# Performance work log

Hardware: AMD Instinct MI355X
Metric: run time of the kernel (lower is better)

Reference implementation:

```python
import jax, jax.numpy as jnp
import numpy as np

B = 256
D = 2048          # in_channels (shared latent dim)
S = 8             # n_subjects
OUT = 1000        # sum of 7 Schaefer network head widths [150,148,132,136,76,122,236]


def setup_inputs() -> dict:
    key = jax.random.key(0)
    k1, k2, k3, k4 = jax.random.split(key, 4)
    x = jax.random.normal(k1, (B, D), dtype=jnp.float32)
    subject_ids = jax.random.randint(k2, (B,), 0, S, dtype=jnp.int64)
    scale = 1.0 / np.sqrt(D)  # matches normal_(0, 1/in_channels**0.5)
    # Concatenated per-head weights: equivalent to 7 heads of shapes
    # (S, D, n_k) concatenated along the output axis (n_k sums to OUT).
    W = jax.random.normal(k3, (S, D, OUT), dtype=jnp.float32) * scale
    b = jax.random.normal(k4, (S, OUT), dtype=jnp.float32) * scale
    return {"x": x, "subject_ids": subject_ids, "W": W, "b": b}


def reference(x, subject_ids, W, b):
    # Per-sample weight gather (B, D, OUT) followed by batched matmul,
    # exactly mirroring torch: w = weights[subject_ids]; einsum('bd,bdo->bo').
    w = W[subject_ids]                      # (B, D, OUT) gathered copy
    out = jnp.einsum('bd,bdo->bo', x, w)    # (B, OUT)
    out = out + b[subject_ids]              # per-subject bias
    return out
```

## Files before the change

### kernel.cpp

```cpp
#include <hip/hip_runtime.h>
#include <stdint.h>

#define Bn   256
#define Dn   2048
#define Sn   8
#define ON   1000

#define ROWS 64
#define OT   32
#define KC   256
#define NDC  (Dn / KC)
#define LDK  (KC + 8)

typedef short v8s __attribute__((ext_vector_type(8)));
typedef float v4f __attribute__((ext_vector_type(4)));

static __device__ __forceinline__ short f2bf(float f) {
    union { float f; uint32_t u; } v; v.f = f;
    uint32_t u = v.u;
    u += 0x7FFFu + ((u >> 16) & 1u);
    return (short)(u >> 16);
}

__global__ __launch_bounds__(256, 3) void main_kernel(const float* __restrict__ x,
                                                      const int* __restrict__ sid,
                                                      const float* __restrict__ W,
                                                      float* __restrict__ part) {
    __shared__ unsigned short Ash[ROWS * LDK];
    __shared__ unsigned short Bsh[OT * LDK];
    __shared__ unsigned long long bmask[4];
    __shared__ int rows_l[ROWS];

    const int s  = blockIdx.x;
    const int oc = blockIdx.y;
    const int dc = blockIdx.z;
    const int o0 = oc * OT;
    const int d0 = dc * KC;
    const int t  = threadIdx.x;
    const int lane = t & 63;
    const int wave = t >> 6;

    const bool match = (sid[t] == s);
    const unsigned long long m = __ballot(match);
    if (lane == 0) bmask[wave] = m;
    if (t < ROWS) rows_l[t] = -1;
    __syncthreads();
    if (match) {
        int pos = __popcll(m & ((1ull << lane) - 1ull));
        for (int w = 0; w < wave; ++w) pos += __popcll(bmask[w]);
        if (pos < ROWS) rows_l[pos] = t;
    }
    __syncthreads();

    const int arow = t >> 2;
    const int ag   = t & 3;
    const int xrow = rows_l[arow];
    const float* xp = (xrow >= 0) ? (x + (size_t)xrow * Dn + d0 + ag * 8) : x;
    const int aoff = arow * LDK + ag * 8;

    int og = o0 + (t & 31); if (og > ON - 1) og = ON - 1;
    const int kg = t >> 5;
    const float* wp = W + (size_t)s * Dn * ON + (size_t)(d0 + kg * 8) * ON + og;
    const int boff = (t & 31) * LDK + kg * 8;

    float4 a[16];
#pragma unroll
    for (int j = 0; j < 8; j++) {
        a[2*j]   = *(const float4*)(xp + j * 32);
        a[2*j+1] = *(const float4*)(xp + j * 32 + 4);
    }
    float b[32];
#pragma unroll
    for (int g = 0; g < 4; g++)
#pragma unroll
        for (int e = 0; e < 8; e++)
            b[g*8+e] = wp[(size_t)(g * 64 + e) * ON];

#pragma unroll
    for (int j = 0; j < 8; j++) {
        const float4 f0 = a[2*j], f1 = a[2*j+1];
        v8s av;
        av[0] = f2bf(f0.x); av[1] = f2bf(f0.y); av[2] = f2bf(f0.z); av[3] = f2bf(f0.w);
        av[4] = f2bf(f1.x); av[5] = f2bf(f1.y); av[6] = f2bf(f1.z); av[7] = f2bf(f1.w);
        *(v8s*)&Ash[aoff + j * 32] = av;
    }
#pragma unroll
    for (int g = 0; g < 4; g++) {
        v8s bv;
#pragma unroll
        for (int e = 0; e < 8; e++) bv[e] = f2bf(b[g*8+e]);
        *(v8s*)&Bsh[boff + g * 64] = bv;
    }

    __syncthreads();

    const int lo16 = lane & 15;
    const int quad = lane >> 4;
    const int ar_off = (wave * 16 + lo16) * LDK;

    v4f acc[2];
    acc[0] = (v4f){0.f, 0.f, 0.f, 0.f};
    acc[1] = (v4f){0.f, 0.f, 0.f, 0.f};

#pragma unroll
    for (int it = 0; it < 8; ++it) {
        const v8s af = *(const v8s*)&Ash[ar_off + it * 32 + quad * 8];
#pragma unroll
        for (int nt = 0; nt < 2; nt++) {
            const v8s bf = *(const v8s*)&Bsh[(nt * 16 + lo16) * LDK + it * 32 + quad * 8];
            acc[nt] = __builtin_amdgcn_mfma_f32_16x16x32_bf16(af, bf, acc[nt], 0, 0, 0);
        }
    }

    float* pp = part + (size_t)dc * Bn * ON;
    const int er0 = wave * 16 + quad * 4;
#pragma unroll
    for (int nt = 0; nt < 2; nt++) {
        const int o = o0 + nt * 16 + lo16;
        if (o < ON) {
#pragma unroll
            for (int r = 0; r < 4; r++) {
                const int bi = rows_l[er0 + r];
                if (bi >= 0) pp[(size_t)bi * ON + o] = acc[nt][r];
            }
        }
    }
}

__global__ __launch_bounds__(256) void reduce_kernel(const int* __restrict__ sid,
                                                     const float* __restrict__ bias,
                                                     const float* __restrict__ part,
                                                     float* __restrict__ out) {
    const int b = blockIdx.x;
    const int s = sid[b];
    const int o = threadIdx.x * 4;
    if (o < ON) {
        float4 v = *(const float4*)(bias + (size_t)s * ON + o);
#pragma unroll
        for (int d = 0; d < NDC; d++) {
            const float4 p = *(const float4*)(part + ((size_t)d * Bn + b) * ON + o);
            v.x += p.x; v.y += p.y; v.z += p.z; v.w += p.w;
        }
        *(float4*)(out + (size_t)b * ON + o) = v;
    }
}

extern "C" void kernel_launch(void* const* d_in, const int* in_sizes, int n_in,
                              void* d_out, int out_size, void* d_ws, size_t ws_size,
                              hipStream_t stream) {
    const float* x    = (const float*)d_in[0];
    const int*   sid  = (const int*)d_in[1];
    const float* W    = (const float*)d_in[2];
    const float* bias = (const float*)d_in[3];
    float*       out  = (float*)d_out;
    float*       part = (float*)d_ws;

    main_kernel<<<dim3(Sn, 32, NDC), dim3(256), 0, stream>>>(x, sid, W, part);
    reduce_kernel<<<dim3(Bn), dim3(256), 0, stream>>>(sid, bias, part, out);
}
```

Before: 113.5 us.

## Load activation fragments directly into registers, dropping the A shared-memory tile

Removes the shared-memory staging buffer for the gathered x rows. Each lane now loads its own MFMA A-fragment straight from global memory, converts it to bf16 in registers, and prefetches the next k-step's fragment one iteration ahead. The W loading is reorganized into two 16-row halves with contiguous 32-element k ranges per thread group, and the occupancy hint is raised from 3 to 4 blocks. This lowers LDS footprint and removes the A-tile write/read round trip, at the cost of more scattered global loads and conversion work inside the MFMA loop.

Measured after the change: 115.7 us. About the same (+1.9%).

```diff
diff --git a/kernel.cpp b/kernel.cpp
--- a/kernel.cpp
+++ b/kernel.cpp
@@ -10,7 +10,7 @@
 #define OT   32
 #define KC   256
 #define NDC  (Dn / KC)
-#define LDK  (KC + 8)
+#define LDK  264
 
 typedef short v8s __attribute__((ext_vector_type(8)));
 typedef float v4f __attribute__((ext_vector_type(4)));
@@ -22,11 +22,17 @@
     return (short)(u >> 16);
 }
 
-__global__ __launch_bounds__(256, 3) void main_kernel(const float* __restrict__ x,
+static __device__ __forceinline__ v8s cvt8(float4 f0, float4 f1) {
+    v8s r;
+    r[0] = f2bf(f0.x); r[1] = f2bf(f0.y); r[2] = f2bf(f0.z); r[3] = f2bf(f0.w);
+    r[4] = f2bf(f1.x); r[5] = f2bf(f1.y); r[6] = f2bf(f1.z); r[7] = f2bf(f1.w);
+    return r;
+}
+
+__global__ __launch_bounds__(256, 4) void main_kernel(const float* __restrict__ x,
                                                       const int* __restrict__ sid,
                                                       const float* __restrict__ W,
                                                       float* __restrict__ part) {
-    __shared__ unsigned short Ash[ROWS * LDK];
     __shared__ unsigned short Bsh[OT * LDK];
     __shared__ unsigned long long bmask[4];
     __shared__ int rows_l[ROWS];
@@ -52,51 +58,35 @@
     }
     __syncthreads();
 
-    const int arow = t >> 2;
-    const int ag   = t & 3;
-    const int xrow = rows_l[arow];
-    const float* xp = (xrow >= 0) ? (x + (size_t)xrow * Dn + d0 + ag * 8) : x;
-    const int aoff = arow * LDK + ag * 8;
-
     int og = o0 + (t & 31); if (og > ON - 1) og = ON - 1;
     const int kg = t >> 5;
-    const float* wp = W + (size_t)s * Dn * ON + (size_t)(d0 + kg * 8) * ON + og;
-    const int boff = (t & 31) * LDK + kg * 8;
-
-    float4 a[16];
-#pragma unroll
-    for (int j = 0; j < 8; j++) {
-        a[2*j]   = *(const float4*)(xp + j * 32);
-        a[2*j+1] = *(const float4*)(xp + j * 32 + 4);
-    }
-    float b[32];
-#pragma unroll
-    for (int g = 0; g < 4; g++)
-#pragma unroll
-        for (int e = 0; e < 8; e++)
-            b[g*8+e] = wp[(size_t)(g * 64 + e) * ON];
+    const float* wp = W + (size_t)s * Dn * ON + (size_t)(d0 + kg * 32) * ON + og;
+    const int boff = (t & 31) * LDK + kg * 32;
 
 #pragma unroll
-    for (int j = 0; j < 8; j++) {
-        const float4 f0 = a[2*j], f1 = a[2*j+1];
-        v8s av;
-        av[0] = f2bf(f0.x); av[1] = f2bf(f0.y); av[2] = f2bf(f0.z); av[3] = f2bf(f0.w);
-        av[4] = f2bf(f1.x); av[5] = f2bf(f1.y); av[6] = f2bf(f1.z); av[7] = f2bf(f1.w);
-        *(v8s*)&Ash[aoff + j * 32] = av;
+    for (int h = 0; h < 2; h++) {
+        float b[16];
+#pragma unroll
+        for (int j = 0; j < 16; j++) b[j] = wp[(size_t)(h * 16 + j) * ON];
+#pragma unroll
+        for (int g = 0; g < 2; g++) {
+            v8s bv;
+#pragma unroll
+            for (int e = 0; e < 8; e++) bv[e] = f2bf(b[g * 8 + e]);
+            *(v8s*)&Bsh[boff + h * 16 + g * 8] = bv;
+        }
     }
-#pragma unroll
-    for (int g = 0; g < 4; g++) {
-        v8s bv;
-#pragma unroll
-        for (int e = 0; e < 8; e++) bv[e] = f2bf(b[g*8+e]);
-        *(v8s*)&Bsh[boff + g * 64] = bv;
-    }
-
-    __syncthreads();
 
     const int lo16 = lane & 15;
     const int quad = lane >> 4;
-    const int ar_off = (wave * 16 + lo16) * LDK;
+    const int arow = rows_l[wave * 16 + lo16];
+    const float* xr = (arow >= 0) ? (x + (size_t)arow * Dn + d0 + quad * 8)
+                                  : (x + d0 + quad * 8);
+
+    float4 p0 = *(const float4*)(xr);
+    float4 p1 = *(const float4*)(xr + 4);
+
+    __syncthreads();
 
     v4f acc[2];
     acc[0] = (v4f){0.f, 0.f, 0.f, 0.f};
@@ -104,7 +94,12 @@
 
 #pragma unroll
     for (int it = 0; it < 8; ++it) {
-        const v8s af = *(const v8s*)&Ash[ar_off + it * 32 + quad * 8];
+        const float4 c0 = p0, c1 = p1;
+        if (it < 7) {
+            p0 = *(const float4*)(xr + (it + 1) * 32);
+            p1 = *(const float4*)(xr + (it + 1) * 32 + 4);
+        }
+        const v8s af = cvt8(c0, c1);
 #pragma unroll
         for (int nt = 0; nt < 2; nt++) {
             const v8s bf = *(const v8s*)&Bsh[(nt * 16 + lo16) * LDK + it * 32 + quad * 8];
```

## Widen output tile to 128, halve K chunk, and load W with float4 rows

Applied to the files above, without the earlier changes.

Each block now covers 128 output columns and 128 of the reduction dimension instead of 32 and 256. W is loaded as coalesced float4 along the output axis and transposed into LDS with scalar bf16 stores, and each wave runs 8 MFMA accumulators per step. The aim is to replace the scalar strided W loads with wide coalesced ones and to reuse each A fragment across more MFMAs. In exchange, the partial buffer written to global memory and read back by the reduce kernel doubles, and the scalar LDS transpose stores with a padded stride of 138 may cause bank conflicts.

Result: no change. 115.3 us (+1.6%).

```diff
diff --git a/kernel.cpp b/kernel.cpp
--- a/kernel.cpp
+++ b/kernel.cpp
@@ -7,10 +7,10 @@
 #define ON   1000
 
 #define ROWS 64
-#define OT   32
-#define KC   256
+#define OT   128
+#define KC   128
 #define NDC  (Dn / KC)
-#define LDK  (KC + 8)
+#define LDK  138
 
 typedef short v8s __attribute__((ext_vector_type(8)));
 typedef float v4f __attribute__((ext_vector_type(4)));
@@ -52,44 +52,41 @@
     }
     __syncthreads();
 
+    const int l = t & 31;
+    const int g = t >> 5;
+    int ob = o0 + l * 4; if (ob > ON - 4) ob = ON - 4;
+    const float* wpB = W + (size_t)s * Dn * ON + (size_t)(d0 + g * 16) * ON + ob;
+
+    float4 bv[16];
+#pragma unroll
+    for (int r = 0; r < 16; r++) bv[r] = *(const float4*)(wpB + (size_t)r * ON);
+
     const int arow = t >> 2;
     const int ag   = t & 3;
     const int xrow = rows_l[arow];
-    const float* xp = (xrow >= 0) ? (x + (size_t)xrow * Dn + d0 + ag * 8) : x;
-    const int aoff = arow * LDK + ag * 8;
-
-    int og = o0 + (t & 31); if (og > ON - 1) og = ON - 1;
-    const int kg = t >> 5;
-    const float* wp = W + (size_t)s * Dn * ON + (size_t)(d0 + kg * 8) * ON + og;
-    const int boff = (t & 31) * LDK + kg * 8;
-
-    float4 a[16];
+    const float* xp = (xrow >= 0) ? (x + (size_t)xrow * Dn + d0 + ag * 32)
+                                  : (x + d0 + ag * 32);
+    float4 av[8];
 #pragma unroll
-    for (int j = 0; j < 8; j++) {
-        a[2*j]   = *(const float4*)(xp + j * 32);
-        a[2*j+1] = *(const float4*)(xp + j * 32 + 4);
-    }
-    float b[32];
-#pragma unroll
-    for (int g = 0; g < 4; g++)
-#pragma unroll
-        for (int e = 0; e < 8; e++)
-            b[g*8+e] = wp[(size_t)(g * 64 + e) * ON];
+    for (int j = 0; j < 8; j++) av[j] = *(const float4*)(xp + j * 4);
 
 #pragma unroll
-    for (int j = 0; j < 8; j++) {
-        const float4 f0 = a[2*j], f1 = a[2*j+1];
-        v8s av;
-        av[0] = f2bf(f0.x); av[1] = f2bf(f0.y); av[2] = f2bf(f0.z); av[3] = f2bf(f0.w);
-        av[4] = f2bf(f1.x); av[5] = f2bf(f1.y); av[6] = f2bf(f1.z); av[7] = f2bf(f1.w);
-        *(v8s*)&Ash[aoff + j * 32] = av;
+    for (int r = 0; r < 16; r++) {
+        const int kk = g * 16 + r;
+        const float4 v = bv[r];
+        Bsh[(l * 4 + 0) * LDK + kk] = (unsigned short)f2bf(v.x);
+        Bsh[(l * 4 + 1) * LDK + kk] = (unsigned short)f2bf(v.y);
+        Bsh[(l * 4 + 2) * LDK + kk] = (unsigned short)f2bf(v.z);
+        Bsh[(l * 4 + 3) * LDK + kk] = (unsigned short)f2bf(v.w);
     }
+
 #pragma unroll
-    for (int g = 0; g < 4; g++) {
-        v8s bv;
-#pragma unroll
-        for (int e = 0; e < 8; e++) bv[e] = f2bf(b[g*8+e]);
-        *(v8s*)&Bsh[boff + g * 64] = bv;
+    for (int h = 0; h < 4; h++) {
+        const float4 f0 = av[2 * h], f1 = av[2 * h + 1];
+        v8s aw;
+        aw[0] = f2bf(f0.x); aw[1] = f2bf(f0.y); aw[2] = f2bf(f0.z); aw[3] = f2bf(f0.w);
+        aw[4] = f2bf(f1.x); aw[5] = f2bf(f1.y); aw[6] = f2bf(f1.z); aw[7] = f2bf(f1.w);
+        *(v8s*)&Ash[arow * LDK + ag * 32 + h * 8] = aw;
     }
 
     __syncthreads();
@@ -98,15 +95,15 @@
     const int quad = lane >> 4;
     const int ar_off = (wave * 16 + lo16) * LDK;
 
-    v4f acc[2];
-    acc[0] = (v4f){0.f, 0.f, 0.f, 0.f};
-    acc[1] = (v4f){0.f, 0.f, 0.f, 0.f};
+    v4f acc[8];
+#pragma unroll
+    for (int i = 0; i < 8; i++) acc[i] = (v4f){0.f, 0.f, 0.f, 0.f};
 
 #pragma unroll
-    for (int it = 0; it < 8; ++it) {
+    for (int it = 0; it < 4; ++it) {
         const v8s af = *(const v8s*)&Ash[ar_off + it * 32 + quad * 8];
 #pragma unroll
-        for (int nt = 0; nt < 2; nt++) {
+        for (int nt = 0; nt < 8; nt++) {
             const v8s bf = *(const v8s*)&Bsh[(nt * 16 + lo16) * LDK + it * 32 + quad * 8];
             acc[nt] = __builtin_amdgcn_mfma_f32_16x16x32_bf16(af, bf, acc[nt], 0, 0, 0);
         }
@@ -115,7 +112,7 @@
     float* pp = part + (size_t)dc * Bn * ON;
     const int er0 = wave * 16 + quad * 4;
 #pragma unroll
-    for (int nt = 0; nt < 2; nt++) {
+    for (int nt = 0; nt < 8; nt++) {
         const int o = o0 + nt * 16 + lo16;
         if (o < ON) {
 #pragma unroll
@@ -155,6 +152,6 @@
     float*       out  = (float*)d_out;
     float*       part = (float*)d_ws;
 
-    main_kernel<<<dim3(Sn, 32, NDC), dim3(256), 0, stream>>>(x, sid, W, part);
+    main_kernel<<<dim3(Sn, 8, NDC), dim3(256), 0, stream>>>(x, sid, W, part);
     reduce_kernel<<<dim3(Bn), dim3(256), 0, stream>>>(sid, bias, part, out);
 }
```
